# Kernel tuning notes

Hardware: AMD Instinct MI355X
Metric: run time of the kernel (lower is better)

The kernel has to match this reference:

```python
import jax, jax.numpy as jnp
import numpy as np

EMBED_DIM = 768
NUM_HEADS = 12
HEAD_DIM = EMBED_DIM // NUM_HEADS


def setup_inputs() -> dict:
    key = jax.random.key(0)
    k_x, k_qkv, k_w, k_b = jax.random.split(key, 4)
    B, N, D = 1, 4096, EMBED_DIM
    scale = 1.0 / np.sqrt(D)
    x = jax.random.normal(k_x, (B, N, D), dtype=jnp.float32)
    # nn.Linear weights: stored as [out, in]; we apply x @ W.T
    w_qkv = jax.random.normal(k_qkv, (3 * D, D), dtype=jnp.float32) * scale
    w_out = jax.random.normal(k_w, (D, D), dtype=jnp.float32) * scale
    b_out = jax.random.normal(k_b, (D,), dtype=jnp.float32) * 0.01
    return {"x": x, "w_qkv": w_qkv, "w_out": w_out, "b_out": b_out}


def reference(x, w_qkv, w_out, b_out):
    B, N, D = x.shape
    H, Hd = NUM_HEADS, HEAD_DIM
    qkv = (x @ w_qkv.T).reshape(B, N, 3, H, Hd)
    q, k, v = qkv[:, :, 0], qkv[:, :, 1], qkv[:, :, 2]
    scores = jnp.einsum('bnhd,bmhd->bhnm', q, k) / jnp.sqrt(jnp.float32(Hd))
    attn = jax.nn.softmax(scores, axis=-1)
    out = jnp.einsum('bhnm,bmhd->bnhd', attn, v).reshape(B, N, D)
    return out @ w_out.T + b_out
```

## Files before the change

kernel.cpp:

```cpp
#include <hip/hip_runtime.h>


typedef __attribute__((ext_vector_type(8))) short short8;
typedef __attribute__((ext_vector_type(4))) float f32x4;

#define N_TOK 4096
#define NHEAD 12
#define DMODEL 768
#define QK_LD 1536

#if defined(__has_builtin)
#if __has_builtin(__builtin_amdgcn_exp2f)
#define EXP2F __builtin_amdgcn_exp2f
#else
#define EXP2F exp2f
#endif
#else
#define EXP2F exp2f
#endif

#if defined(__has_builtin)
#if __has_builtin(__builtin_amdgcn_perm)
#define PACK2BF(hi, lo) __builtin_amdgcn_perm((hi), (lo), 0x07060302u)
#else
#define PACK2BF(hi, lo) ((((hi)) & 0xffff0000u) | (((lo)) >> 16))
#endif
#else
#define PACK2BF(hi, lo) ((((hi)) & 0xffff0000u) | (((lo)) >> 16))
#endif

__device__ __forceinline__ ushort bf16bits(float x) {
  union { float f; unsigned u; } cv; cv.f = x;
  unsigned u = cv.u;
  u += 0x7fffu + ((u >> 16) & 1u);
  return (ushort)(u >> 16);
}
__device__ __forceinline__ float bf2f(ushort u) {
  return __uint_as_float(((unsigned)u) << 16);
}

__device__ __forceinline__ void async16(ushort* lds, const ushort* g) {
  __builtin_amdgcn_global_load_lds((const __attribute__((address_space(1))) unsigned int*)g,
                                   (__attribute__((address_space(3))) unsigned int*)lds,
                                   16, 0, 0);
}

__global__ void __launch_bounds__(256) cvt3(const float* __restrict__ x,
                                            const float* __restrict__ wq,
                                            const float* __restrict__ wo,
                                            ushort* __restrict__ xb,
                                            ushort* __restrict__ wqb,
                                            ushort* __restrict__ wob) {
  const int b = blockIdx.x, t = threadIdx.x;
  const float* src; ushort* dst; int i;
  if (b < 3072)      { src = x;  dst = xb;  i = b * 256 + t; }
  else if (b < 4800) { src = wq; dst = wqb; i = (b - 3072) * 256 + t; }
  else               { src = wo; dst = wob; i = (b - 4800) * 256 + t; }
  const float4 v = ((const float4*)src)[i];
  ushort4 o;
  o.x = bf16bits(v.x); o.y = bf16bits(v.y); o.z = bf16bits(v.z); o.w = bf16bits(v.w);
  ((ushort4*)dst)[i] = o;
}

#define GEMM_STAGE96(Ms, Mp, MK)                                               \
  do {                                                                         \
    _Pragma("unroll")                                                          \
    for (int i_ = 0; i_ < 3; i_++)                                             \
      async16(&(Ms)[(wave * 24 + i_ * 8) * 64],                                \
              Mp + (size_t)(wave * 24 + i_ * 8 + lrow) * (MK) + lcol);         \
  } while (0)

#define GEMM_STAGE64(Ms, Mp, MK)                                               \
  do {                                                                         \
    _Pragma("unroll")                                                          \
    for (int i_ = 0; i_ < 2; i_++)                                             \
      async16(&(Ms)[(wave * 16 + i_ * 8) * 64],                                \
              Mp + (size_t)(wave * 16 + i_ * 8 + lrow) * (MK) + lcol);         \
  } while (0)

__global__ void __launch_bounds__(256) gemm_qkv(const ushort* __restrict__ A,
                                                const ushort* __restrict__ B,
                                                ushort* __restrict__ qkb,
                                                ushort* __restrict__ vtg) {
  __shared__ __align__(16) ushort As[2][64 * 64];
  __shared__ __align__(16) ushort Bs[2][96 * 64];
  const int tid = threadIdx.x;
  const int wave = tid >> 6, lane = tid & 63, quad = lane >> 4, l16 = lane & 15;
  const int wm = wave & 1, wn = wave >> 1;
  const int lrow = lane >> 3, lcol = (lane & 7) * 8;
  const int m0 = blockIdx.y * 64, n0 = blockIdx.x * 96;
  const int K = DMODEL;

  f32x4 acc[2][3] = {};
  const ushort* Ap = A + (size_t)m0 * K;
  const ushort* Bp = B + (size_t)n0 * K;

  GEMM_STAGE64(As[0], Ap, K);
  GEMM_STAGE96(Bs[0], Bp, K);
  __syncthreads();

  for (int k0 = 0; k0 < K; k0 += 64) {
    const int cur = (k0 >> 6) & 1, nxt = cur ^ 1;
    if (k0 + 64 < K) {
      GEMM_STAGE64(As[nxt], Ap + k0 + 64, K);
      GEMM_STAGE96(Bs[nxt], Bp + k0 + 64, K);
    }
#pragma unroll
    for (int ks = 0; ks < 2; ks++) {
      short8 af[2], bf[3];
#pragma unroll
      for (int i = 0; i < 2; i++)
        af[i] = *(const short8*)&As[cur][(wm * 32 + i * 16 + l16) * 64 + ks * 32 + quad * 8];
#pragma unroll
      for (int i = 0; i < 3; i++)
        bf[i] = *(const short8*)&Bs[cur][(wn * 48 + i * 16 + l16) * 64 + ks * 32 + quad * 8];
#pragma unroll
      for (int mi = 0; mi < 2; mi++)
#pragma unroll
        for (int ni = 0; ni < 3; ni++)
          acc[mi][ni] = __builtin_amdgcn_mfma_f32_16x16x32_bf16(af[mi], bf[ni], acc[mi][ni], 0, 0, 0);
    }
    __syncthreads();
  }

  if (n0 < QK_LD) {
    const float qsc = (n0 < 768) ? 0.18033688011112042f : 1.0f;
#pragma unroll
    for (int mi = 0; mi < 2; mi++)
#pragma unroll
      for (int ni = 0; ni < 3; ni++) {
        const int col = n0 + wn * 48 + ni * 16 + l16;
#pragma unroll
        for (int rr = 0; rr < 4; rr++) {
          const int row = m0 + wm * 32 + mi * 16 + quad * 4 + rr;
          qkb[(size_t)row * QK_LD + col] = bf16bits(acc[mi][ni][rr] * qsc);
        }
      }
  } else {
#pragma unroll
    for (int mi = 0; mi < 2; mi++)
#pragma unroll
      for (int ni = 0; ni < 3; ni++) {
        const int col = n0 + wn * 48 + ni * 16 + l16 - QK_LD;
        const int rowb = m0 + wm * 32 + mi * 16 + quad * 4;
        const unsigned u0 = (unsigned)bf16bits(acc[mi][ni][0]) |
                            ((unsigned)bf16bits(acc[mi][ni][1]) << 16);
        const unsigned u1 = (unsigned)bf16bits(acc[mi][ni][2]) |
                            ((unsigned)bf16bits(acc[mi][ni][3]) << 16);
        *(uint2*)&vtg[(size_t)col * N_TOK + rowb] = make_uint2(u0, u1);
      }
  }
}

__global__ void __launch_bounds__(256) gemm_out(const ushort* __restrict__ A,
                                                const ushort* __restrict__ B,
                                                float* __restrict__ Cf,
                                                const float* __restrict__ bias) {
  __shared__ __align__(16) ushort As[2][64 * 64];
  __shared__ __align__(16) ushort Bs[2][64 * 64];
  const int tid = threadIdx.x;
  const int wave = tid >> 6, lane = tid & 63, quad = lane >> 4, l16 = lane & 15;
  const int wm = wave & 1, wn = wave >> 1;
  const int lrow = lane >> 3, lcol = (lane & 7) * 8;
  const int m0 = blockIdx.y * 64, n0 = blockIdx.x * 64;
  const int K = DMODEL, Nn = DMODEL;

  f32x4 acc[2][2] = {};
  const ushort* Ap = A + (size_t)m0 * K;
  const ushort* Bp = B + (size_t)n0 * K;

  GEMM_STAGE64(As[0], Ap, K);
  GEMM_STAGE64(Bs[0], Bp, K);
  __syncthreads();

  for (int k0 = 0; k0 < K; k0 += 64) {
    const int cur = (k0 >> 6) & 1, nxt = cur ^ 1;
    if (k0 + 64 < K) {
      GEMM_STAGE64(As[nxt], Ap + k0 + 64, K);
      GEMM_STAGE64(Bs[nxt], Bp + k0 + 64, K);
    }
#pragma unroll
    for (int ks = 0; ks < 2; ks++) {
      short8 af[2], bf[2];
#pragma unroll
      for (int i = 0; i < 2; i++) {
        af[i] = *(const short8*)&As[cur][(wm * 32 + i * 16 + l16) * 64 + ks * 32 + quad * 8];
        bf[i] = *(const short8*)&Bs[cur][(wn * 32 + i * 16 + l16) * 64 + ks * 32 + quad * 8];
      }
#pragma unroll
      for (int mi = 0; mi < 2; mi++)
#pragma unroll
        for (int ni = 0; ni < 2; ni++)
          acc[mi][ni] = __builtin_amdgcn_mfma_f32_16x16x32_bf16(af[mi], bf[ni], acc[mi][ni], 0, 0, 0);
    }
    __syncthreads();
  }

#pragma unroll
  for (int mi = 0; mi < 2; mi++)
#pragma unroll
    for (int ni = 0; ni < 2; ni++) {
      const int col = n0 + wn * 32 + ni * 16 + l16;
#pragma unroll
      for (int rr = 0; rr < 4; rr++) {
        const int row = m0 + wm * 32 + mi * 16 + quad * 4 + rr;
        Cf[(size_t)row * Nn + col] = acc[mi][ni][rr] + bias[col];
      }
    }
}


#define ATTN_STAGE(bufi)                                                       \
  do {                                                                         \
    async16(&Ks[bufi][(wave * 16) * 64],     kp0);                             \
    async16(&Ks[bufi][(wave * 16 + 8) * 64], kp1);                             \
    async16(&Vs[bufi][(wave * 16) * 64],     vp0);                             \
    async16(&Vs[bufi][(wave * 16 + 8) * 64], vp1);                             \
    kp0 += (size_t)64 * QK_LD; kp1 += (size_t)64 * QK_LD;                      \
    vp0 += 64; vp1 += 64;                                                      \
  } while (0)

#define WAITBAR4()                                                             \
  do {                                                                         \
    asm volatile("s_waitcnt vmcnt(4) lgkmcnt(0)" ::: "memory");                \
    __builtin_amdgcn_s_barrier();                                              \
  } while (0)

#define WAITBAR0()                                                             \
  do {                                                                         \
    asm volatile("s_waitcnt vmcnt(0) lgkmcnt(0)" ::: "memory");                \
    __builtin_amdgcn_s_barrier();                                              \
  } while (0)

#define ATTN_TILE(KbP, VbP)                                                    \
  do {                                                                         \
    const ushort* Kb_ = (KbP);                                                 \
    const ushort* Vb_ = (VbP);                                                 \
    _Pragma("unroll")                                                          \
    for (int ks = 0; ks < 2; ks++) {                                           \
      union { unsigned u[4]; short8 v; } pfu0, pfu1;                           \
      _Pragma("unroll")                                                        \
      for (int h2 = 0; h2 < 2; h2++) {                                         \
        const int nt = 2 * ks + h2;                                            \
        const short8 kf0 = *(const short8*)&Kb_[(nt * 16 + l16) * 64 + u0];    \
        const short8 kf1 = *(const short8*)&Kb_[(nt * 16 + l16) * 64 + u1];    \
        f32x4 a0 = __builtin_amdgcn_mfma_f32_16x16x32_bf16(kf0, qf[0][0], z4, 0, 0, 0); \
        a0 = __builtin_amdgcn_mfma_f32_16x16x32_bf16(kf1, qf[0][1], a0, 0, 0, 0);       \
        f32x4 a1 = __builtin_amdgcn_mfma_f32_16x16x32_bf16(kf0, qf[1][0], z4, 0, 0, 0); \
        a1 = __builtin_amdgcn_mfma_f32_16x16x32_bf16(kf1, qf[1][1], a1, 0, 0, 0);       \
        {                                                                      \
          const float e0 = EXP2F(a0[0]);                                       \
          const float e1 = EXP2F(a0[1]);                                       \
          const float e2 = EXP2F(a0[2]);                                       \
          const float e3 = EXP2F(a0[3]);                                       \
          lsum[0] += (e0 + e1) + (e2 + e3);                                    \
          pfu0.u[2 * h2]     = PACK2BF(__float_as_uint(e1), __float_as_uint(e0)); \
          pfu0.u[2 * h2 + 1] = PACK2BF(__float_as_uint(e3), __float_as_uint(e2)); \
        }                                                                      \
        {                                                                      \
          const float e0 = EXP2F(a1[0]);                                       \
          const float e1 = EXP2F(a1[1]);                                       \
          const float e2 = EXP2F(a1[2]);                                       \
          const float e3 = EXP2F(a1[3]);                                       \
          lsum[1] += (e0 + e1) + (e2 + e3);                                    \
          pfu1.u[2 * h2]     = PACK2BF(__float_as_uint(e1), __float_as_uint(e0)); \
          pfu1.u[2 * h2 + 1] = PACK2BF(__float_as_uint(e3), __float_as_uint(e2)); \
        }                                                                      \
      }                                                                        \
      const short8 pf0 = pfu0.v, pf1 = pfu1.v;                                 \
      _Pragma("unroll")                                                        \
      for (int dt = 0; dt < 4; dt++) {                                         \
        const short8 vf = *(const short8*)&Vb_[(dt * 16 + l16) * 64 + (ks ? u1 : u0)]; \
        o[0][dt] = __builtin_amdgcn_mfma_f32_16x16x32_bf16(pf0, vf, o[0][dt], 0, 0, 0); \
        o[1][dt] = __builtin_amdgcn_mfma_f32_16x16x32_bf16(pf1, vf, o[1][dt], 0, 0, 0); \
      }                                                                        \
    }                                                                          \
  } while (0)

__global__ void __launch_bounds__(256, 3) attn_flash(const ushort* __restrict__ qk,
                                                     const ushort* __restrict__ vtg,
                                                     ushort* __restrict__ pob,
                                                     float* __restrict__ pl,
                                                     int ntiles, int nsl8) {
  __shared__ __align__(16) ushort Ks[3][64 * 64];
  __shared__ __align__(16) ushort Vs[3][64 * 64];

  const int b = blockIdx.x;
  const int s8 = b & 7;
  const int j = b >> 3;
  const int slice = s8 + 8 * (j % nsl8);
  const int qb = j / nsl8;
  const int h = slice % NHEAD;
  const int sp = slice / NHEAD;

  const int tid = threadIdx.x;
  const int wave = tid >> 6, lane = tid & 63, quad = lane >> 4, l16 = lane & 15;
  const int q0 = qb * 128 + wave * 32;

  short8 qf[2][2];
#pragma unroll
  for (int s = 0; s < 2; s++) {
    const ushort* qp = qk + (size_t)(q0 + s * 16 + l16) * QK_LD + h * 64 + quad * 8;
    qf[s][0] = *(const short8*)qp;
    qf[s][1] = *(const short8*)(qp + 32);
  }

  const int srow = wave * 16 + (lane >> 3);
  const int un = (((lane & 7) ^ (lane >> 3)) * 8);
  const int g0 = ((srow >> 5) << 5) + (((srow >> 2) & 3) << 3) +
                 (((srow >> 4) & 1) << 2) + (srow & 3);
  const int kt0 = sp * ntiles;
  const ushort* kp0 = qk + 768 + h * 64 + un + (size_t)(kt0 * 64 + g0) * QK_LD;
  const ushort* kp1 = kp0 + (size_t)16 * QK_LD;
  const ushort* vp0 = vtg + (size_t)(h * 64 + srow) * N_TOK + kt0 * 64 + un;
  const ushort* vp1 = vp0 + (size_t)8 * N_TOK;

  const int u0 = (quad ^ (l16 & 7)) * 8;
  const int u1 = u0 ^ 32;

  f32x4 o[2][4] = {};
  float lsum[2] = {};
  const f32x4 z4 = {};

  ATTN_STAGE(0);
  ATTN_STAGE(1);
  WAITBAR4();

  int bc = 0;
  int bs = 2;
  for (int kt = 0; kt < ntiles; kt++) {
    const bool more = (kt + 2 < ntiles);
    if (more) ATTN_STAGE(bs);
    ATTN_TILE(Ks[bc], Vs[bc]);
    if (more) WAITBAR4(); else WAITBAR0();
    bc = (bc == 2) ? 0 : bc + 1;
    bs = (bs == 2) ? 0 : bs + 1;
  }

#pragma unroll
  for (int s = 0; s < 2; s++) {
    float lt = lsum[s];
    lt += __shfl_xor(lt, 16, 64);
    lt += __shfl_xor(lt, 32, 64);
#pragma unroll
    for (int rr = 0; rr < 4; rr++) {
      const float l = __shfl(lt, quad * 16 + quad * 4 + rr, 64);
      const float inv = 1.f / l;
      const int row = q0 + s * 16 + quad * 4 + rr;
      if (l16 == 0)
        pl[(size_t)(sp * NHEAD + h) * N_TOK + row] = l;
#pragma unroll
      for (int dt = 0; dt < 4; dt++)
        pob[((size_t)sp * N_TOK + row) * DMODEL + h * 64 + dt * 16 + l16] =
            bf16bits(o[s][dt][rr] * inv);
    }
  }
}

__global__ void __launch_bounds__(256) combine(const ushort* __restrict__ pob,
                                               const float* __restrict__ pl,
                                               ushort* __restrict__ aout, int S) {
  const int i = blockIdx.x * 256 + threadIdx.x;
  const int row = i / (DMODEL / 4);
  const int hd = (i % (DMODEL / 4)) * 4;
  const int h = hd >> 6;
  float lt = 0.f, a0 = 0.f, a1 = 0.f, a2 = 0.f, a3 = 0.f;
  for (int s = 0; s < S; s++) {
    const float l = pl[((size_t)s * NHEAD + h) * N_TOK + row];
    const ushort4 a = *(const ushort4*)&pob[((size_t)s * N_TOK + row) * DMODEL + hd];
    lt += l;
    a0 += l * bf2f(a.x); a1 += l * bf2f(a.y); a2 += l * bf2f(a.z); a3 += l * bf2f(a.w);
  }
  const float inv = 1.f / lt;
  ushort4 r;
  r.x = bf16bits(a0 * inv); r.y = bf16bits(a1 * inv);
  r.z = bf16bits(a2 * inv); r.w = bf16bits(a3 * inv);
  *(ushort4*)&aout[(size_t)row * DMODEL + hd] = r;
}

extern "C" void kernel_launch(void* const* d_in, const int* in_sizes, int n_in,
                              void* d_out, int out_size, void* d_ws, size_t ws_size,
                              hipStream_t stream) {
  const float* x     = (const float*)d_in[0];
  const float* w_qkv = (const float*)d_in[1];
  const float* w_out = (const float*)d_in[2];
  const float* b_out = (const float*)d_in[3];
  float* out = (float*)d_out;

  const size_t PO_UNIT = 6291456UL;
  const int S = (ws_size >= 4 * PO_UNIT + 20840448UL) ? 4 : 2;
  char* ws = (char*)d_ws;
  ushort* pob   = (ushort*)ws;
  ushort* xb    = (ushort*)ws;
  ushort* wqkvb = (ushort*)(ws + 6291456UL);
  ushort* qkb   = (ushort*)(ws + (size_t)S * PO_UNIT);
  ushort* vtg   = (ushort*)((char*)qkb + 12582912UL);
  ushort* woutb = (ushort*)((char*)vtg + 6291456UL);
  float*  pl    = (float*)((char*)woutb + 1179648UL);
  ushort* aoutb = qkb;

  cvt3<<<5376, 256, 0, stream>>>(x, w_qkv, w_out, xb, wqkvb, woutb);

  gemm_qkv<<<dim3(24, 64), 256, 0, stream>>>(xb, wqkvb, qkb, vtg);

  attn_flash<<<384 * S, 256, 0, stream>>>(qkb, vtg, pob, pl, 64 / S, (12 * S) / 8);

  combine<<<3072, 256, 0, stream>>>(pob, pl, aoutb, S);

  gemm_out<<<dim3(12, 64), 256, 0, stream>>>(aoutb, woutb, out, b_out);
}
```

Baseline: 186.1 us.

## Triple-buffer GEMM loads with vmcnt waits and shrink QKV tile to 64

```diff
diff --git a/kernel.cpp b/kernel.cpp
--- a/kernel.cpp
+++ b/kernel.cpp
@@ -44,6 +44,18 @@
                                    (__attribute__((address_space(3))) unsigned int*)lds,
                                    16, 0, 0);
 }
+
+#define WAITBAR4()                                                             \
+  do {                                                                         \
+    asm volatile("s_waitcnt vmcnt(4) lgkmcnt(0)" ::: "memory");                \
+    __builtin_amdgcn_s_barrier();                                              \
+  } while (0)
+
+#define WAITBAR0()                                                             \
+  do {                                                                         \
+    asm volatile("s_waitcnt vmcnt(0) lgkmcnt(0)" ::: "memory");                \
+    __builtin_amdgcn_s_barrier();                                              \
+  } while (0)
 
 __global__ void __launch_bounds__(256) cvt3(const float* __restrict__ x,
                                             const float* __restrict__ wq,
@@ -62,14 +74,6 @@
   ((ushort4*)dst)[i] = o;
 }
 
-#define GEMM_STAGE96(Ms, Mp, MK)                                               \
-  do {                                                                         \
-    _Pragma("unroll")                                                          \
-    for (int i_ = 0; i_ < 3; i_++)                                             \
-      async16(&(Ms)[(wave * 24 + i_ * 8) * 64],                                \
-              Mp + (size_t)(wave * 24 + i_ * 8 + lrow) * (MK) + lcol);         \
-  } while (0)
-
 #define GEMM_STAGE64(Ms, Mp, MK)                                               \
   do {                                                                         \
     _Pragma("unroll")                                                          \
@@ -82,45 +86,49 @@
                                                 const ushort* __restrict__ B,
                                                 ushort* __restrict__ qkb,
                                                 ushort* __restrict__ vtg) {
-  __shared__ __align__(16) ushort As[2][64 * 64];
-  __shared__ __align__(16) ushort Bs[2][96 * 64];
+  __shared__ __align__(16) ushort As[3][64 * 64];
+  __shared__ __align__(16) ushort Bs[3][64 * 64];
   const int tid = threadIdx.x;
   const int wave = tid >> 6, lane = tid & 63, quad = lane >> 4, l16 = lane & 15;
   const int wm = wave & 1, wn = wave >> 1;
   const int lrow = lane >> 3, lcol = (lane & 7) * 8;
-  const int m0 = blockIdx.y * 64, n0 = blockIdx.x * 96;
+  const int m0 = blockIdx.y * 64, n0 = blockIdx.x * 64;
   const int K = DMODEL;
 
-  f32x4 acc[2][3] = {};
+  f32x4 acc[2][2] = {};
   const ushort* Ap = A + (size_t)m0 * K;
   const ushort* Bp = B + (size_t)n0 * K;
 
   GEMM_STAGE64(As[0], Ap, K);
-  GEMM_STAGE96(Bs[0], Bp, K);
-  __syncthreads();
-
+  GEMM_STAGE64(Bs[0], Bp, K);
+  GEMM_STAGE64(As[1], Ap + 64, K);
+  GEMM_STAGE64(Bs[1], Bp + 64, K);
+  WAITBAR4();
+
+  int bc = 0, bs = 2;
   for (int k0 = 0; k0 < K; k0 += 64) {
-    const int cur = (k0 >> 6) & 1, nxt = cur ^ 1;
-    if (k0 + 64 < K) {
-      GEMM_STAGE64(As[nxt], Ap + k0 + 64, K);
-      GEMM_STAGE96(Bs[nxt], Bp + k0 + 64, K);
+    const bool more = (k0 + 128 < K);
+    if (more) {
+      GEMM_STAGE64(As[bs], Ap + k0 + 128, K);
+      GEMM_STAGE64(Bs[bs], Bp + k0 + 128, K);
     }
 #pragma unroll
     for (int ks = 0; ks < 2; ks++) {
-      short8 af[2], bf[3];
-#pragma unroll
-      for (int i = 0; i < 2; i++)
-        af[i] = *(const short8*)&As[cur][(wm * 32 + i * 16 + l16) * 64 + ks * 32 + quad * 8];
-#pragma unroll
-      for (int i = 0; i < 3; i++)
-        bf[i] = *(const short8*)&Bs[cur][(wn * 48 + i * 16 + l16) * 64 + ks * 32 + quad * 8];
+      short8 af[2], bf[2];
+#pragma unroll
+      for (int i = 0; i < 2; i++) {
+        af[i] = *(const short8*)&As[bc][(wm * 32 + i * 16 + l16) * 64 + ks * 32 + quad * 8];
+        bf[i] = *(const short8*)&Bs[bc][(wn * 32 + i * 16 + l16) * 64 + ks * 32 + quad * 8];
+      }
 #pragma unroll
       for (int mi = 0; mi < 2; mi++)
 #pragma unroll
-        for (int ni = 0; ni < 3; ni++)
+        for (int ni = 0; ni < 2; ni++)
           acc[mi][ni] = __builtin_amdgcn_mfma_f32_16x16x32_bf16(af[mi], bf[ni], acc[mi][ni], 0, 0, 0);
     }
-    __syncthreads();
+    if (more) WAITBAR4(); else WAITBAR0();
+    bc = (bc == 2) ? 0 : bc + 1;
+    bs = (bs == 2) ? 0 : bs + 1;
   }
 
   if (n0 < QK_LD) {
@@ -128,8 +136,8 @@
 #pragma unroll
     for (int mi = 0; mi < 2; mi++)
 #pragma unroll
-      for (int ni = 0; ni < 3; ni++) {
-        const int col = n0 + wn * 48 + ni * 16 + l16;
+      for (int ni = 0; ni < 2; ni++) {
+        const int col = n0 + wn * 32 + ni * 16 + l16;
 #pragma unroll
         for (int rr = 0; rr < 4; rr++) {
           const int row = m0 + wm * 32 + mi * 16 + quad * 4 + rr;
@@ -140,8 +148,8 @@
 #pragma unroll
     for (int mi = 0; mi < 2; mi++)
 #pragma unroll
-      for (int ni = 0; ni < 3; ni++) {
-        const int col = n0 + wn * 48 + ni * 16 + l16 - QK_LD;
+      for (int ni = 0; ni < 2; ni++) {
+        const int col = n0 + wn * 32 + ni * 16 + l16 - QK_LD;
         const int rowb = m0 + wm * 32 + mi * 16 + quad * 4;
         const unsigned u0 = (unsigned)bf16bits(acc[mi][ni][0]) |
                             ((unsigned)bf16bits(acc[mi][ni][1]) << 16);
@@ -156,8 +164,8 @@
                                                 const ushort* __restrict__ B,
                                                 float* __restrict__ Cf,
                                                 const float* __restrict__ bias) {
-  __shared__ __align__(16) ushort As[2][64 * 64];
-  __shared__ __align__(16) ushort Bs[2][64 * 64];
+  __shared__ __align__(16) ushort As[3][64 * 64];
+  __shared__ __align__(16) ushort Bs[3][64 * 64];
   const int tid = threadIdx.x;
   const int wave = tid >> 6, lane = tid & 63, quad = lane >> 4, l16 = lane & 15;
   const int wm = wave & 1, wn = wave >> 1;
@@ -171,21 +179,24 @@
 
   GEMM_STAGE64(As[0], Ap, K);
   GEMM_STAGE64(Bs[0], Bp, K);
-  __syncthreads();
-
+  GEMM_STAGE64(As[1], Ap + 64, K);
+  GEMM_STAGE64(Bs[1], Bp + 64, K);
+  WAITBAR4();
+
+  int bc = 0, bs = 2;
   for (int k0 = 0; k0 < K; k0 += 64) {
-    const int cur = (k0 >> 6) & 1, nxt = cur ^ 1;
-    if (k0 + 64 < K) {
-      GEMM_STAGE64(As[nxt], Ap + k0 + 64, K);
-      GEMM_STAGE64(Bs[nxt], Bp + k0 + 64, K);
+    const bool more = (k0 + 128 < K);
+    if (more) {
+      GEMM_STAGE64(As[bs], Ap + k0 + 128, K);
+      GEMM_STAGE64(Bs[bs], Bp + k0 + 128, K);
     }
 #pragma unroll
     for (int ks = 0; ks < 2; ks++) {
       short8 af[2], bf[2];
 #pragma unroll
       for (int i = 0; i < 2; i++) {
-        af[i] = *(const short8*)&As[cur][(wm * 32 + i * 16 + l16) * 64 + ks * 32 + quad * 8];
-        bf[i] = *(const short8*)&Bs[cur][(wn * 32 + i * 16 + l16) * 64 + ks * 32 + quad * 8];
+        af[i] = *(const short8*)&As[bc][(wm * 32 + i * 16 + l16) * 64 + ks * 32 + quad * 8];
+        bf[i] = *(const short8*)&Bs[bc][(wn * 32 + i * 16 + l16) * 64 + ks * 32 + quad * 8];
       }
 #pragma unroll
       for (int mi = 0; mi < 2; mi++)
@@ -193,7 +204,9 @@
         for (int ni = 0; ni < 2; ni++)
           acc[mi][ni] = __builtin_amdgcn_mfma_f32_16x16x32_bf16(af[mi], bf[ni], acc[mi][ni], 0, 0, 0);
     }
-    __syncthreads();
+    if (more) WAITBAR4(); else WAITBAR0();
+    bc = (bc == 2) ? 0 : bc + 1;
+    bs = (bs == 2) ? 0 : bs + 1;
   }
 
 #pragma unroll
@@ -218,18 +231,6 @@
     async16(&Vs[bufi][(wave * 16 + 8) * 64], vp1);                             \
     kp0 += (size_t)64 * QK_LD; kp1 += (size_t)64 * QK_LD;                      \
     vp0 += 64; vp1 += 64;                                                      \
-  } while (0)
-
-#define WAITBAR4()                                                             \
-  do {                                                                         \
-    asm volatile("s_waitcnt vmcnt(4) lgkmcnt(0)" ::: "memory");                \
-    __builtin_amdgcn_s_barrier();                                              \
-  } while (0)
-
-#define WAITBAR0()                                                             \
-  do {                                                                         \
-    asm volatile("s_waitcnt vmcnt(0) lgkmcnt(0)" ::: "memory");                \
-    __builtin_amdgcn_s_barrier();                                              \
   } while (0)
 
 #define ATTN_TILE(KbP, VbP)                                                    \
@@ -401,7 +402,7 @@
 
   cvt3<<<5376, 256, 0, stream>>>(x, w_qkv, w_out, xb, wqkvb, woutb);
 
-  gemm_qkv<<<dim3(24, 64), 256, 0, stream>>>(xb, wqkvb, qkb, vtg);
+  gemm_qkv<<<dim3(36, 64), 256, 0, stream>>>(xb, wqkvb, qkb, vtg);
 
   attn_flash<<<384 * S, 256, 0, stream>>>(qkb, vtg, pob, pl, 64 / S, (12 * S) / 8);
 
```

New measurement: 193.5 us. 1.04x slower.
